# Kernel tuning notes

Measured on AMD Instinct MI355X. Metric: run time of the kernel, lower is better.

The kernel has to match this reference:

```python
import jax, jax.numpy as jnp
import numpy as np

B, S, H = 2, 2048, 1024
NH, HD = 16, 64
WINDOW = 512
NEG = -10000.0


def setup_inputs() -> dict:
    key = jax.random.key(0)
    ks = jax.random.split(key, 8)
    sc = 0.02
    return {
        "hidden_states": jax.random.normal(ks[0], (B, S, H), dtype=jnp.float32),
        "attention_mask": jnp.zeros((B, 1, 1, S), dtype=jnp.float32),
        "Wq": jax.random.normal(ks[1], (H, H), dtype=jnp.float32) * sc,
        "bq": jnp.zeros((H,), dtype=jnp.float32),
        "Wk": jax.random.normal(ks[2], (H, H), dtype=jnp.float32) * sc,
        "bk": jnp.zeros((H,), dtype=jnp.float32),
        "Wv": jax.random.normal(ks[3], (H, H), dtype=jnp.float32) * sc,
        "bv": jnp.zeros((H,), dtype=jnp.float32),
    }


def _heads(x):
    # [b, t, (h d)] -> [b, h, t, d]
    b, t, _ = x.shape
    return x.reshape(b, t, NH, HD).transpose(0, 2, 1, 3)


def reference(hidden_states, attention_mask, Wq, bq, Wk, bk, Wv, bv):
    q = _heads(hidden_states @ Wq.T + bq)
    k = _heads(hidden_states @ Wk.T + bk)
    v = _heads(hidden_states @ Wv.T + bv)

    # Faithful mask construction (note: window mask is triu(diag=-WINDOW),
    # penalizing the recent window, exactly as in the source).
    i = jnp.arange(S)[:, None]
    j = jnp.arange(S)[None, :]
    causal_mask = jnp.where(j > i, NEG, 0.0).astype(jnp.float32)          # triu, diag=1
    window_mask = jnp.where(j >= i - WINDOW, NEG, 0.0).astype(jnp.float32)  # triu, diag=-512
    mask = causal_mask + window_mask + attention_mask  # [b,1,S,S]

    scale = 1.0 / jnp.sqrt(jnp.asarray(HD, dtype=q.dtype))
    scores = jnp.einsum("bhtd,bhsd->bhts", q, k) * scale + mask  # [b,h,S,S]
    probs = jax.nn.softmax(scores, axis=-1)
    out = jnp.einsum("bhts,bhsd->bhtd", probs, v)  # [b,h,S,d]
    # [b,h,t,d] -> [b,t,(h d)]
    return out.transpose(0, 2, 1, 3).reshape(B, S, H)
```

## Files before the change

### kernel.cpp

```cpp
#include <hip/hip_runtime.h>

typedef float f32x2 __attribute__((ext_vector_type(2)));
typedef float f32x4 __attribute__((ext_vector_type(4)));
typedef float f32x16 __attribute__((ext_vector_type(16)));
typedef _Float16 half8 __attribute__((ext_vector_type(8)));
typedef _Float16 half4 __attribute__((ext_vector_type(4)));
typedef unsigned int u32;
typedef u32 u32x4 __attribute__((ext_vector_type(4)));

#define S_LEN 2048
#define NHEAD 16
#define HDIM 64
#define BATCH 2
#define WINDOW 512
#define M2_FIX 5.770780163555852f
#define LOG2E 1.4426950408889634f

#define GLDS16(gp, lp) __builtin_amdgcn_global_load_lds( \
    (const __attribute__((address_space(1))) void*)(gp), \
    (__attribute__((address_space(3))) void*)(lp), 16, 0, 0)


__global__ __launch_bounds__(256) void convert_kernel(
    const float4* __restrict__ hs, const float4* __restrict__ wq,
    const float4* __restrict__ wk, const float4* __restrict__ wv,
    _Float16* __restrict__ hsb, _Float16* __restrict__ wb) {
  int i = blockIdx.x * 256 + threadIdx.x;
  float4 v;
  _Float16* dst;
  if (i < 1048576) {
    v = hs[i];
    dst = hsb + (size_t)i * 4;
  } else {
    int j = i - 1048576;
    if (j < 262144) v = wq[j];
    else if (j < 524288) v = wk[j - 262144];
    else v = wv[j - 524288];
    dst = wb + (size_t)j * 4;
  }
  half4 o;
  o[0] = (_Float16)v.x; o[1] = (_Float16)v.y;
  o[2] = (_Float16)v.z; o[3] = (_Float16)v.w;
  *(half4*)dst = o;
}

__global__ __launch_bounds__(512, 2) void qkv_gemm(
    const _Float16* __restrict__ A, const _Float16* __restrict__ W,
    const float* __restrict__ bq, const float* __restrict__ bk,
    const float* __restrict__ bv,
    _Float16* __restrict__ Qf, _Float16* __restrict__ Kf, _Float16* __restrict__ Vf) {
  __shared__ _Float16 sbuf[65536];
  const int tid = threadIdx.x;
  const int wv = tid >> 6;
  const int lane = tid & 63;
  const int g = lane >> 4;
  const int c = lane & 15;
  const int bid = blockIdx.x;
  const int m0 = (bid & 15) * 256;
  const int n0 = (bid >> 4) * 256;
  const int wm = wv >> 2;
  const int wn = wv & 3;

  const int srow = tid >> 3;
  const int sk = ((tid & 7) ^ ((tid >> 3) & 7)) * 8;
  const _Float16* aSrc = A + (size_t)(m0 + srow) * 1024 + sk;
  const _Float16* bSrc = W + (size_t)(n0 + srow) * 1024 + sk;
  char* const ldsB = (char*)&sbuf[0];

  auto STAGE_A = [&](int bf_, int k0, int grp) __attribute__((always_inline)) {
    GLDS16(aSrc + (size_t)grp * 65536 + k0,
           ldsB + bf_ * 32768 + grp * 8192 + tid * 16);
  };
  auto STAGE_B = [&](int bf_, int k0, int grp) __attribute__((always_inline)) {
    GLDS16(bSrc + (size_t)grp * 65536 + k0,
           ldsB + 65536 + bf_ * 32768 + grp * 8192 + tid * 16);
  };

  const int slot0 = ((0 * 4 + g) ^ (c & 7)) * 8;
  const int slot1 = ((4 + g) ^ (c & 7)) * 8;
  const int aRow = wm * 128 + c;
  const int bRow = wn * 64 + c;

  f32x4 acc[8][4];
#pragma unroll
  for (int i = 0; i < 8; ++i)
#pragma unroll
    for (int j = 0; j < 4; ++j) acc[i][j] = (f32x4){0.f, 0.f, 0.f, 0.f};

#pragma unroll
  for (int grp = 0; grp < 4; ++grp) STAGE_A(0, 0, grp);
#pragma unroll
  for (int grp = 0; grp < 4; ++grp) STAGE_B(0, 0, grp);
  asm volatile("s_waitcnt vmcnt(0)" ::: "memory");
  __builtin_amdgcn_sched_barrier(0);
  __builtin_amdgcn_s_barrier();

#define READA(dstv, ph)                                                       \
  {                                                                           \
    _Pragma("unroll") for (int mi = 0; mi < 2; ++mi) {                        \
      const int row = aRow + (2 * (ph) + mi) * 16;                            \
      dstv[mi][0] = *(const half8*)&sbuf[abase + row * 64 + slot0];           \
      dstv[mi][1] = *(const half8*)&sbuf[abase + row * 64 + slot1];           \
    }                                                                         \
  }
#define MFMAP(ph, srcv)                                                       \
  {                                                                           \
    __builtin_amdgcn_s_setprio(1);                                            \
    _Pragma("unroll") for (int nf = 0; nf < 4; ++nf)                          \
        _Pragma("unroll") for (int mi = 0; mi < 2; ++mi) {                    \
      acc[2 * (ph) + mi][nf] = __builtin_amdgcn_mfma_f32_16x16x32_f16(        \
          srcv[mi][0], bfr[nf][0], acc[2 * (ph) + mi][nf], 0, 0, 0);          \
      acc[2 * (ph) + mi][nf] = __builtin_amdgcn_mfma_f32_16x16x32_f16(        \
          srcv[mi][1], bfr[nf][1], acc[2 * (ph) + mi][nf], 0, 0, 0);          \
    }                                                                         \
    __builtin_amdgcn_s_setprio(0);                                            \
  }

  half8 bfr[4][2], aqA[2][2], aqB[2][2];
  for (int t = 0; t < 16; ++t) {
    const int bf = t & 1;
    const int abase = bf * 16384;
    const int bbase = 32768 + bf * 16384;
    const int kn = (t + 1) * 64;
    const bool st = t < 15;

#pragma unroll
    for (int nf = 0; nf < 4; ++nf) {
      bfr[nf][0] = *(const half8*)&sbuf[bbase + (bRow + nf * 16) * 64 + slot0];
      bfr[nf][1] = *(const half8*)&sbuf[bbase + (bRow + nf * 16) * 64 + slot1];
    }
    READA(aqA, 0);
    if (st) {
      STAGE_A(bf ^ 1, kn, 0); STAGE_A(bf ^ 1, kn, 1);
      STAGE_A(bf ^ 1, kn, 2); STAGE_A(bf ^ 1, kn, 3);
    }
    READA(aqB, 1);
    MFMAP(0, aqA);
    if (st) {
      STAGE_B(bf ^ 1, kn, 0); STAGE_B(bf ^ 1, kn, 1);
      STAGE_B(bf ^ 1, kn, 2); STAGE_B(bf ^ 1, kn, 3);
    }
    READA(aqA, 2);
    MFMAP(1, aqB);
    READA(aqB, 3);
    MFMAP(2, aqA);
    MFMAP(3, aqB);

    asm volatile("s_waitcnt vmcnt(0)" ::: "memory");
    __builtin_amdgcn_sched_barrier(0);
    __builtin_amdgcn_s_barrier();
  }

  const int nAbs = n0 + wn * 64;
  const int kind = nAbs >> 10;
  const int nb = nAbs & 1023;
  const int head = nb >> 6;
  const float* bias = kind == 0 ? bq : (kind == 1 ? bk : bv);
  _Float16* dst = kind == 0 ? Qf : (kind == 1 ? Kf : Vf);
  _Float16* ob = &sbuf[wv * 8192];

  if (kind < 2) {
    const float scl = kind == 0 ? (0.125f * LOG2E) : 1.0f;
#pragma unroll
    for (int nf = 0; nf < 4; ++nf) {
      const int d = nf * 16 + c;
      const float bsv = bias[nb + d];
      const int base = nf * 512 + ((c >> 3) & 1) * 256 + (c & 7);
#pragma unroll
      for (int mf = 0; mf < 8; ++mf) {
#pragma unroll
        for (int r = 0; r < 4; ++r) {
          ob[(mf >> 1) * 2048 + base + (mf & 1) * 128 + g * 32 + r * 8] =
              (_Float16)((acc[mf][nf][r] + bsv) * scl);
        }
      }
    }
  } else {
#pragma unroll
    for (int nf = 0; nf < 4; ++nf) {
      const int d = nf * 16 + c;
      const float bsv = bias[nb + d];
#pragma unroll
      for (int mf = 0; mf < 8; ++mf) {
        half4 v4;
#pragma unroll
        for (int r = 0; r < 4; ++r) v4[r] = (_Float16)(acc[mf][nf][r] + bsv);
        *(half4*)&ob[(mf >> 1) * 2048 + ((nf >> 1) * 2 + (mf & 1)) * 512 +
                     ((g >> 1) * 32 + (nf & 1) * 16 + c) * 8 + (g & 1) * 4] = v4;
      }
    }
  }

  const int mRow = m0 + wm * 128;
  const int bI = mRow >> 11;
  const size_t gbase = (size_t)(bI * NHEAD + head) * 131072 +
                       (size_t)((mRow & 2047) >> 5) * 2048;
#pragma unroll
  for (int i = 0; i < 16; ++i) {
    half8 v = *(const half8*)&ob[i * 512 + lane * 8];
    *(half8*)&dst[gbase + i * 512 + lane * 8] = v;
  }
}

__global__ __launch_bounds__(256) void attn_kernel(
    const _Float16* __restrict__ Qf, const _Float16* __restrict__ Kf,
    const _Float16* __restrict__ Vf, const float* __restrict__ amask,
    float* __restrict__ out) {
  __shared__ _Float16 obuf[4][32][72];
  __shared__ float lbuf[4][32];
  const int tid = threadIdx.x;
  const int w = tid >> 6;
  const int lane = tid & 63;
  const int q31 = lane & 31;
  const int h = lane >> 5;
  const int bid = blockIdx.x;
  const int bh = bid & 31;
  const int idx = 63 - (bid >> 5);
  const int i0 = idx * 32;
  const int bI = bh >> 4;
  const int head = bh & 15;

  const _Float16* Qh = Qf + (size_t)bh * 131072;
  const _Float16* Kh = Kf + (size_t)bh * 131072;
  const _Float16* Vh = Vf + (size_t)bh * 131072;
  const float* am = amask + (size_t)bI * S_LEN;

  const int q = i0 + q31;
  const int hiq = (q <= WINDOW) ? q : (q - WINDOW - 1);
  const int last = i0 + 31;
  const int himax = (last <= WINDOW) ? last
                    : ((i0 <= WINDOW) ? WINDOW : (last - WINDOW - 1));
  const int hiq_min = (last <= WINDOW) ? i0
                      : ((i0 > WINDOW) ? (i0 - WINDOW - 1) : 0);
  const int ntiles = (himax >> 5) + 1;
  const int nfull = (hiq_min + 1) >> 5;
  const int lim = hiq - 4 * h;

  half8 qf[4];
#pragma unroll
  for (int ch = 0; ch < 4; ++ch)
    qf[ch] = *(const half8*)&Qh[(size_t)idx * 2048 + ch * 512 + lane * 8];

  f32x16 zero16, m2init;
#pragma unroll
  for (int r = 0; r < 16; ++r) { zero16[r] = 0.f; m2init[r] = -M2_FIX; }
  f32x16 oacc0 = zero16, oacc1 = zero16;
  f32x2 lp[4];
#pragma unroll
  for (int r = 0; r < 4; ++r) lp[r] = (f32x2){0.f, 0.f};

  auto computeTile = [&](half8 k0, half8 k1, half8 k2, half8 k3,
                         half8 vf0, half8 vf1, half8 vf2, half8 vf3,
                         f32x4 am0, f32x4 am1, f32x4 am2, f32x4 am3, int t)
      __attribute__((always_inline)) {
    const int j0 = t * 32;
    f32x4 amv[4] = {am0, am1, am2, am3};

    __builtin_amdgcn_s_setprio(1);
    f32x16 st = __builtin_amdgcn_mfma_f32_32x32x16_f16(k0, qf[0], m2init, 0, 0, 0);
    st = __builtin_amdgcn_mfma_f32_32x32x16_f16(k1, qf[1], st, 0, 0, 0);
    st = __builtin_amdgcn_mfma_f32_32x32x16_f16(k2, qf[2], st, 0, 0, 0);
    st = __builtin_amdgcn_mfma_f32_32x32x16_f16(k3, qf[3], st, 0, 0, 0);
    __builtin_amdgcn_s_setprio(0);

    float p[16];
#pragma unroll
    for (int r = 0; r < 16; ++r)
      p[r] = __builtin_fmaf(amv[r >> 2][r & 3], LOG2E, st[r]);
    if (t >= nfull) {
      const int lm = lim - j0;
#pragma unroll
      for (int r = 0; r < 16; ++r) {
        const int off = (r & 3) + 8 * (r >> 2);
        p[r] = (off <= lm) ? p[r] : -3e38f;
      }
    }
#pragma unroll
    for (int r = 0; r < 16; ++r) p[r] = __builtin_amdgcn_exp2f(p[r]);
#pragma unroll
    for (int j = 0; j < 4; ++j) {
      lp[j] += (f32x2){p[2 * j], p[2 * j + 1]};
      lp[j] += (f32x2){p[8 + 2 * j], p[9 + 2 * j]};
    }

    u32 pk[8];
#pragma unroll
    for (int r = 0; r < 8; ++r) {
      auto c2 = __builtin_amdgcn_cvt_pkrtz(p[2 * r], p[2 * r + 1]);
      pk[r] = __builtin_bit_cast(u32, c2);
    }
    u32 a0 = pk[0], b0 = pk[2];
    u32 a1 = pk[1], b1 = pk[3];
    u32 a2 = pk[4], b2 = pk[6];
    u32 a3 = pk[5], b3 = pk[7];
    asm("v_permlane32_swap_b32 %0, %1" : "+v"(a0), "+v"(b0));
    asm("v_permlane32_swap_b32 %0, %1" : "+v"(a1), "+v"(b1));
    asm("v_permlane32_swap_b32 %0, %1" : "+v"(a2), "+v"(b2));
    asm("v_permlane32_swap_b32 %0, %1" : "+v"(a3), "+v"(b3));
    const half8 pf0 = __builtin_bit_cast(half8, (u32x4){a0, a1, b0, b1});
    const half8 pf1 = __builtin_bit_cast(half8, (u32x4){a2, a3, b2, b3});

    __builtin_amdgcn_s_setprio(1);
    oacc0 = __builtin_amdgcn_mfma_f32_32x32x16_f16(vf0, pf0, oacc0, 0, 0, 0);
    oacc0 = __builtin_amdgcn_mfma_f32_32x32x16_f16(vf1, pf1, oacc0, 0, 0, 0);
    oacc1 = __builtin_amdgcn_mfma_f32_32x32x16_f16(vf2, pf0, oacc1, 0, 0, 0);
    oacc1 = __builtin_amdgcn_mfma_f32_32x32x16_f16(vf3, pf1, oacc1, 0, 0, 0);
    __builtin_amdgcn_s_setprio(0);
  };

#define LOADALL(k0, k1, k2, k3, v0, v1, v2, v3, a0_, a1_, a2_, a3_, tt)  \
  {                                                                      \
    const _Float16* kt = Kh + (size_t)(tt) * 2048 + lane * 8;            \
    const _Float16* vt = Vh + (size_t)(tt) * 2048 + lane * 8;            \
    const float* at = am + (tt) * 32 + 4 * h;                            \
    k0 = *(const half8*)&kt[0];                                          \
    k1 = *(const half8*)&kt[512];                                        \
    k2 = *(const half8*)&kt[1024];                                       \
    k3 = *(const half8*)&kt[1536];                                       \
    v0 = *(const half8*)&vt[0];                                          \
    v1 = *(const half8*)&vt[512];                                        \
    v2 = *(const half8*)&vt[1024];                                       \
    v3 = *(const half8*)&vt[1536];                                       \
    a0_ = *(const f32x4*)&at[0];                                         \
    a1_ = *(const f32x4*)&at[8];                                         \
    a2_ = *(const f32x4*)&at[16];                                        \
    a3_ = *(const f32x4*)&at[24];                                        \
  }

  int t = w;
  if (t < ntiles) {
    half8 k0, k1, k2, k3, v0, v1, v2, v3;
    f32x4 a0, a1, a2, a3;
    LOADALL(k0, k1, k2, k3, v0, v1, v2, v3, a0, a1, a2, a3, t);
    int tn = t + 4;
    while (tn < ntiles) {
      half8 n0, n1, n2, n3, u0, u1, u2, u3;
      f32x4 e0, e1, e2, e3;
      LOADALL(n0, n1, n2, n3, u0, u1, u2, u3, e0, e1, e2, e3, tn);
      computeTile(k0, k1, k2, k3, v0, v1, v2, v3, a0, a1, a2, a3, t);
      k0 = n0; k1 = n1; k2 = n2; k3 = n3;
      v0 = u0; v1 = u1; v2 = u2; v3 = u3;
      a0 = e0; a1 = e1; a2 = e2; a3 = e3;
      t = tn;
      tn += 4;
    }
    computeTile(k0, k1, k2, k3, v0, v1, v2, v3, a0, a1, a2, a3, t);
  }

  f32x2 s2 = (lp[0] + lp[1]) + (lp[2] + lp[3]);
  float lw = s2[0] + s2[1];
  lw += __shfl_xor(lw, 32);
  if (h == 0) lbuf[w][q31] = lw;
#pragma unroll
  for (int j = 0; j < 4; ++j) {
    half4 h0, h1;
#pragma unroll
    for (int e = 0; e < 4; ++e) {
      h0[e] = (_Float16)oacc0[4 * j + e];
      h1[e] = (_Float16)oacc1[4 * j + e];
    }
    *(half4*)&obuf[w][q31][4 * h + 8 * j]      = h0;
    *(half4*)&obuf[w][q31][32 + 4 * h + 8 * j] = h1;
  }
  __syncthreads();

  const int mq = tid >> 3;
  const int md = (tid & 7) * 8;
  const float lt = (lbuf[0][mq] + lbuf[1][mq]) + (lbuf[2][mq] + lbuf[3][mq]);
  float s[8];
  half8 p0 = *(const half8*)&obuf[0][mq][md];
#pragma unroll
  for (int e = 0; e < 8; ++e) s[e] = (float)p0[e];
#pragma unroll
  for (int w4 = 1; w4 < 4; ++w4) {
    half8 pw = *(const half8*)&obuf[w4][mq][md];
#pragma unroll
    for (int e = 0; e < 8; ++e) s[e] += (float)pw[e];
  }
  const float inv = 1.0f / lt;
  float4 s0, s1;
  s0.x = s[0] * inv; s0.y = s[1] * inv; s0.z = s[2] * inv; s0.w = s[3] * inv;
  s1.x = s[4] * inv; s1.y = s[5] * inv; s1.z = s[6] * inv; s1.w = s[7] * inv;
  float* op = out + ((size_t)(bI * S_LEN + i0 + mq)) * 1024 + head * 64 + md;
  *(float4*)op = s0;
  *(float4*)(op + 4) = s1;
}

extern "C" void kernel_launch(void* const* d_in, const int* in_sizes, int n_in,
                              void* d_out, int out_size, void* d_ws, size_t ws_size,
                              hipStream_t stream) {
  const float* hs = (const float*)d_in[0];
  const float* am = (const float*)d_in[1];
  const float* Wq = (const float*)d_in[2];
  const float* bq = (const float*)d_in[3];
  const float* Wk = (const float*)d_in[4];
  const float* bk = (const float*)d_in[5];
  const float* Wv = (const float*)d_in[6];
  const float* bv = (const float*)d_in[7];
  float* out = (float*)d_out;

  char* ws = (char*)d_ws;
  _Float16* hsb = (_Float16*)(ws);
  _Float16* wb  = (_Float16*)(ws + 8388608);
  _Float16* Qf  = (_Float16*)(ws + 14680064);
  _Float16* Kf  = (_Float16*)(ws + 23068672);
  _Float16* Vf  = (_Float16*)(ws + 31457280);

  convert_kernel<<<7168, 256, 0, stream>>>(
      (const float4*)hs, (const float4*)Wq, (const float4*)Wk, (const float4*)Wv, hsb, wb);
  qkv_gemm<<<192, 512, 0, stream>>>(hsb, wb, bq, bk, bv, Qf, Kf, Vf);
  attn_kernel<<<2048, 256, 0, stream>>>(Qf, Kf, Vf, am, out);
}
```

Before: 69.95 us.

## Process two KV tiles per iteration to interleave QK MFMAs with softmax

Restructures the attention inner loop to handle two key tiles per iteration. Both QK products are issued back-to-back, then both softmax blocks, then both PV products, with next K tiles prefetched early and V/mask loaded inside the iteration. An odd leading tile is peeled off. The aim is to hide MFMA latency and the exp/pack dependency chain through more independent work per wave. The cost is higher register pressure and V loads that are no longer prefetched a full iteration ahead.

Measured after the change: 68.16 us. -2.6%, faster.

```diff
diff --git a/kernel.cpp b/kernel.cpp
--- a/kernel.cpp
+++ b/kernel.cpp
@@ -241,34 +241,30 @@
   for (int ch = 0; ch < 4; ++ch)
     qf[ch] = *(const half8*)&Qh[(size_t)idx * 2048 + ch * 512 + lane * 8];
 
-  f32x16 zero16, m2init;
-#pragma unroll
-  for (int r = 0; r < 16; ++r) { zero16[r] = 0.f; m2init[r] = -M2_FIX; }
-  f32x16 oacc0 = zero16, oacc1 = zero16;
+  f32x16 m2init;
+#pragma unroll
+  for (int r = 0; r < 16; ++r) m2init[r] = -M2_FIX;
+  f32x16 oacc0 = {}, oacc1 = {};
   f32x2 lp[4];
 #pragma unroll
   for (int r = 0; r < 4; ++r) lp[r] = (f32x2){0.f, 0.f};
 
-  auto computeTile = [&](half8 k0, half8 k1, half8 k2, half8 k3,
-                         half8 vf0, half8 vf1, half8 vf2, half8 vf3,
-                         f32x4 am0, f32x4 am1, f32x4 am2, f32x4 am3, int t)
+  auto QK = [&](const half8 k[4]) __attribute__((always_inline)) -> f32x16 {
+    __builtin_amdgcn_s_setprio(1);
+    f32x16 st = __builtin_amdgcn_mfma_f32_32x32x16_f16(k[0], qf[0], m2init, 0, 0, 0);
+    st = __builtin_amdgcn_mfma_f32_32x32x16_f16(k[1], qf[1], st, 0, 0, 0);
+    st = __builtin_amdgcn_mfma_f32_32x32x16_f16(k[2], qf[2], st, 0, 0, 0);
+    st = __builtin_amdgcn_mfma_f32_32x32x16_f16(k[3], qf[3], st, 0, 0, 0);
+    __builtin_amdgcn_s_setprio(0);
+    return st;
+  };
+  auto SM = [&](const f32x16& st, const f32x4 amv[4], int t, float p[16])
       __attribute__((always_inline)) {
-    const int j0 = t * 32;
-    f32x4 amv[4] = {am0, am1, am2, am3};
-
-    __builtin_amdgcn_s_setprio(1);
-    f32x16 st = __builtin_amdgcn_mfma_f32_32x32x16_f16(k0, qf[0], m2init, 0, 0, 0);
-    st = __builtin_amdgcn_mfma_f32_32x32x16_f16(k1, qf[1], st, 0, 0, 0);
-    st = __builtin_amdgcn_mfma_f32_32x32x16_f16(k2, qf[2], st, 0, 0, 0);
-    st = __builtin_amdgcn_mfma_f32_32x32x16_f16(k3, qf[3], st, 0, 0, 0);
-    __builtin_amdgcn_s_setprio(0);
-
-    float p[16];
 #pragma unroll
     for (int r = 0; r < 16; ++r)
       p[r] = __builtin_fmaf(amv[r >> 2][r & 3], LOG2E, st[r]);
     if (t >= nfull) {
-      const int lm = lim - j0;
+      const int lm = lim - t * 32;
 #pragma unroll
       for (int r = 0; r < 16; ++r) {
         const int off = (r & 3) + 8 * (r >> 2);
@@ -282,7 +278,9 @@
       lp[j] += (f32x2){p[2 * j], p[2 * j + 1]};
       lp[j] += (f32x2){p[8 + 2 * j], p[9 + 2 * j]};
     }
-
+  };
+  auto PACKF = [&](float p[16], half8& pf0, half8& pf1)
+      __attribute__((always_inline)) {
     u32 pk[8];
 #pragma unroll
     for (int r = 0; r < 8; ++r) {
@@ -297,54 +295,84 @@
     asm("v_permlane32_swap_b32 %0, %1" : "+v"(a1), "+v"(b1));
     asm("v_permlane32_swap_b32 %0, %1" : "+v"(a2), "+v"(b2));
     asm("v_permlane32_swap_b32 %0, %1" : "+v"(a3), "+v"(b3));
-    const half8 pf0 = __builtin_bit_cast(half8, (u32x4){a0, a1, b0, b1});
-    const half8 pf1 = __builtin_bit_cast(half8, (u32x4){a2, a3, b2, b3});
-
+    pf0 = __builtin_bit_cast(half8, (u32x4){a0, a1, b0, b1});
+    pf1 = __builtin_bit_cast(half8, (u32x4){a2, a3, b2, b3});
+  };
+  auto PV = [&](const half8 v[4], half8 pf0, half8 pf1)
+      __attribute__((always_inline)) {
     __builtin_amdgcn_s_setprio(1);
-    oacc0 = __builtin_amdgcn_mfma_f32_32x32x16_f16(vf0, pf0, oacc0, 0, 0, 0);
-    oacc0 = __builtin_amdgcn_mfma_f32_32x32x16_f16(vf1, pf1, oacc0, 0, 0, 0);
-    oacc1 = __builtin_amdgcn_mfma_f32_32x32x16_f16(vf2, pf0, oacc1, 0, 0, 0);
-    oacc1 = __builtin_amdgcn_mfma_f32_32x32x16_f16(vf3, pf1, oacc1, 0, 0, 0);
+    oacc0 = __builtin_amdgcn_mfma_f32_32x32x16_f16(v[0], pf0, oacc0, 0, 0, 0);
+    oacc0 = __builtin_amdgcn_mfma_f32_32x32x16_f16(v[1], pf1, oacc0, 0, 0, 0);
+    oacc1 = __builtin_amdgcn_mfma_f32_32x32x16_f16(v[2], pf0, oacc1, 0, 0, 0);
+    oacc1 = __builtin_amdgcn_mfma_f32_32x32x16_f16(v[3], pf1, oacc1, 0, 0, 0);
     __builtin_amdgcn_s_setprio(0);
   };
 
-#define LOADALL(k0, k1, k2, k3, v0, v1, v2, v3, a0_, a1_, a2_, a3_, tt)  \
+#define LK(d, tt)                                                        \
   {                                                                      \
     const _Float16* kt = Kh + (size_t)(tt) * 2048 + lane * 8;            \
+    d[0] = *(const half8*)&kt[0];                                        \
+    d[1] = *(const half8*)&kt[512];                                      \
+    d[2] = *(const half8*)&kt[1024];                                     \
+    d[3] = *(const half8*)&kt[1536];                                     \
+  }
+#define LV(d, tt)                                                        \
+  {                                                                      \
     const _Float16* vt = Vh + (size_t)(tt) * 2048 + lane * 8;            \
+    d[0] = *(const half8*)&vt[0];                                        \
+    d[1] = *(const half8*)&vt[512];                                      \
+    d[2] = *(const half8*)&vt[1024];                                     \
+    d[3] = *(const half8*)&vt[1536];                                     \
+  }
+#define LAM(d, tt)                                                       \
+  {                                                                      \
     const float* at = am + (tt) * 32 + 4 * h;                            \
-    k0 = *(const half8*)&kt[0];                                          \
-    k1 = *(const half8*)&kt[512];                                        \
-    k2 = *(const half8*)&kt[1024];                                       \
-    k3 = *(const half8*)&kt[1536];                                       \
-    v0 = *(const half8*)&vt[0];                                          \
-    v1 = *(const half8*)&vt[512];                                        \
-    v2 = *(const half8*)&vt[1024];                                       \
-    v3 = *(const half8*)&vt[1536];                                       \
-    a0_ = *(const f32x4*)&at[0];                                         \
-    a1_ = *(const f32x4*)&at[8];                                         \
-    a2_ = *(const f32x4*)&at[16];                                        \
-    a3_ = *(const f32x4*)&at[24];                                        \
+    d[0] = *(const f32x4*)&at[0];                                        \
+    d[1] = *(const f32x4*)&at[8];                                        \
+    d[2] = *(const f32x4*)&at[16];                                       \
+    d[3] = *(const f32x4*)&at[24];                                       \
   }
 
   int t = w;
   if (t < ntiles) {
-    half8 k0, k1, k2, k3, v0, v1, v2, v3;
-    f32x4 a0, a1, a2, a3;
-    LOADALL(k0, k1, k2, k3, v0, v1, v2, v3, a0, a1, a2, a3, t);
-    int tn = t + 4;
-    while (tn < ntiles) {
-      half8 n0, n1, n2, n3, u0, u1, u2, u3;
-      f32x4 e0, e1, e2, e3;
-      LOADALL(n0, n1, n2, n3, u0, u1, u2, u3, e0, e1, e2, e3, tn);
-      computeTile(k0, k1, k2, k3, v0, v1, v2, v3, a0, a1, a2, a3, t);
-      k0 = n0; k1 = n1; k2 = n2; k3 = n3;
-      v0 = u0; v1 = u1; v2 = u2; v3 = u3;
-      a0 = e0; a1 = e1; a2 = e2; a3 = e3;
-      t = tn;
-      tn += 4;
-    }
-    computeTile(k0, k1, k2, k3, v0, v1, v2, v3, a0, a1, a2, a3, t);
+    const int cnt = (ntiles - w + 3) >> 2;
+    half8 kA[4], kB[4], vA[4], vB[4];
+    f32x4 aA[4], aB[4];
+    if (cnt & 1) {
+      LK(kA, t); LV(vA, t); LAM(aA, t);
+      f32x16 st = QK(kA);
+      float p[16];
+      SM(st, aA, t, p);
+      half8 pf0, pf1;
+      PACKF(p, pf0, pf1);
+      PV(vA, pf0, pf1);
+      t += 4;
+    }
+    if (t < ntiles) {
+      LK(kA, t); LK(kB, t + 4);
+      for (;;) {
+        const int tA = t, tB = t + 4;
+        LV(vA, tA); LV(vB, tB); LAM(aA, tA); LAM(aB, tB);
+        f32x16 stA = QK(kA);
+        f32x16 stB = QK(kB);
+        const int tn = t + 8;
+        const bool more = tn < ntiles;
+        half8 nkA[4], nkB[4];
+        if (more) { LK(nkA, tn); LK(nkB, tn + 4); }
+        float pA[16], pB[16];
+        SM(stA, aA, tA, pA);
+        SM(stB, aB, tB, pB);
+        half8 pfA0, pfA1, pfB0, pfB1;
+        PACKF(pA, pfA0, pfA1);
+        PACKF(pB, pfB0, pfB1);
+        PV(vA, pfA0, pfA1);
+        PV(vB, pfB0, pfB1);
+        if (!more) break;
+#pragma unroll
+        for (int e = 0; e < 4; ++e) { kA[e] = nkA[e]; kB[e] = nkB[e]; }
+        t = tn;
+      }
+    }
   }
 
   f32x2 s2 = (lp[0] + lp[1]) + (lp[2] + lp[3]);
```
